# Kernel optimization log

Measured on AMD Instinct MI355X. Metric: run time of the kernel, lower is better.

Reference implementation:

```python
import jax, jax.numpy as jnp
import numpy as np

IN, H, OUT, B = 1024, 4096, 1, 4096


def setup_inputs() -> dict:
    key = jax.random.key(0)
    ks = jax.random.split(key, 20)
    sx = 1.0 / np.sqrt(IN)
    sh = 1.0 / np.sqrt(H)
    d = {
        "x": jax.random.normal(ks[0], (B, IN), jnp.float32),
        "hidden": jax.random.normal(ks[1], (B, H), jnp.float32),
        "cell": jax.random.normal(ks[2], (B, H), jnp.float32),
        # input projections (Linear(input_size, h_size)), weight [H, IN], bias [H]
        "Wx_i": jax.random.normal(ks[3], (H, IN), jnp.float32) * sx,
        "Wx_f": jax.random.normal(ks[4], (H, IN), jnp.float32) * sx,
        "Wx_o": jax.random.normal(ks[5], (H, IN), jnp.float32) * sx,
        "Wx_c": jax.random.normal(ks[6], (H, IN), jnp.float32) * sx,
        "bx_i": jax.random.normal(ks[7], (H,), jnp.float32) * sx,
        "bx_f": jax.random.normal(ks[8], (H,), jnp.float32) * sx,
        "bx_o": jax.random.normal(ks[9], (H,), jnp.float32) * sx,
        "bx_c": jax.random.normal(ks[10], (H,), jnp.float32) * sx,
        # hidden projections (Linear(h_size, h_size, bias=False)), weight [H, H]
        "Wh_i": jax.random.normal(ks[11], (H, H), jnp.float32) * sh,
        "Wh_f": jax.random.normal(ks[12], (H, H), jnp.float32) * sh,
        "Wh_o": jax.random.normal(ks[13], (H, H), jnp.float32) * sh,
        "Wh_c": jax.random.normal(ks[14], (H, H), jnp.float32) * sh,
        # output head Linear(h_size, out_size)
        "Wy": jax.random.normal(ks[15], (OUT, H), jnp.float32) * sh,
        "by": jax.random.normal(ks[16], (OUT,), jnp.float32) * sh,
    }
    return d


def reference(x, hidden, cell,
              Wx_i, Wx_f, Wx_o, Wx_c,
              bx_i, bx_f, bx_o, bx_c,
              Wh_i, Wh_f, Wh_o, Wh_c,
              Wy, by):
    # single LSTM step, batched over leading dim
    i = jax.nn.sigmoid(x @ Wx_i.T + bx_i + hidden @ Wh_i.T)
    f = jax.nn.sigmoid(x @ Wx_f.T + bx_f + hidden @ Wh_f.T)
    o = jax.nn.sigmoid(x @ Wx_o.T + bx_o + hidden @ Wh_o.T)
    c_til = jnp.tanh(x @ Wx_c.T + bx_c + hidden @ Wh_c.T)
    c_new = f * cell + i * c_til
    h_new = o * jnp.tanh(c_new)
    y_hat = h_new @ Wy.T + by  # [B, OUT]
    return y_hat
```

## Files before the change

kernel.cpp:

```cpp
#include <hip/hip_runtime.h>
#include <stdint.h>

#define IN_ 1024
#define H_  4096
#define B_  4096
#define K_  5120
#define NT_ 80

typedef short bf16x8 __attribute__((ext_vector_type(8)));
typedef float f32x4  __attribute__((ext_vector_type(4)));

__device__ __forceinline__ unsigned short f2bf(float x) {
    union { float f; uint32_t u; } v; v.f = x;
    return (unsigned short)((v.u + 0x7FFFu + ((v.u >> 16) & 1u)) >> 16);
}
__device__ __forceinline__ float bf2f(uint32_t u16) {
    union { uint32_t u; float f; } v; v.u = u16 << 16; return v.f;
}

__global__ __launch_bounds__(256) void cvt_cat(
    const float* __restrict__ s1, const float* __restrict__ s2,
    unsigned short* __restrict__ dst)
{
    int idx = blockIdx.x * 256 + threadIdx.x;
    int r = idx / (K_ / 4);
    int c = (idx % (K_ / 4)) * 4;
    float4 v;
    if (c < IN_) v = *(const float4*)(s1 + (size_t)r * IN_ + c);
    else         v = *(const float4*)(s2 + (size_t)r * H_ + (c - IN_));
    ushort4 o = { f2bf(v.x), f2bf(v.y), f2bf(v.z), f2bf(v.w) };
    *(ushort4*)(dst + (size_t)r * K_ + c) = o;
}

__device__ __forceinline__ int swz(int row) { return ((row >> 1) & 3) << 4; }

__global__ __launch_bounds__(512, 2) void gemm_gate8(
    const unsigned short* __restrict__ A,
    const unsigned short* __restrict__ W,
    const float* __restrict__ bias,
    unsigned short* __restrict__ P)
{
    __shared__ __align__(16) char ldsb[131072];

    const int tid  = threadIdx.x;
    const int wid  = tid >> 6;
    const int lane = tid & 63;

    const int wg = (blockIdx.x & 7) * 32 + (blockIdx.x >> 3);
    const int mt = wg & 15, nt = wg >> 4;
    const int bm = mt * 256, bn = nt * 256;

    const int wm = wid >> 2;
    const int wn = wid & 3;

    const int l15 = lane & 15;
    const int c0  = (lane >> 4) << 4;

    const int q0  = wid * 64 + lane;
    const int r0  = q0 >> 2;
    const int cb0 = ((q0 & 3) << 4) ^ swz(r0);
    const int r1  = r0 + 128;
    const int cb1 = ((q0 & 3) << 4) ^ swz(r1);

    f32x4 acc[8][4];
#pragma unroll
    for (int i = 0; i < 8; ++i)
#pragma unroll
        for (int j = 0; j < 4; ++j) acc[i][j] = (f32x4){0.f, 0.f, 0.f, 0.f};

    auto stage = [&](int isB, int ksel, int tau) {
        if (tau >= NT_) tau -= 2;
        const int kbase = tau * 64 + ksel * 32;
        const int chunk = (tau & 1) * 65536 + isB * 32768 + ksel * 16384;
        const unsigned short* src = isB ? W : A;
        const int gb = isB ? bn : bm;
        __builtin_amdgcn_global_load_lds(
            (const __attribute__((address_space(1))) void*)(src + (size_t)(gb + r0) * K_ + kbase + (cb0 >> 1)),
            (__attribute__((address_space(3))) void*)(ldsb + chunk + wid * 1024), 16, 0, 0);
        __builtin_amdgcn_global_load_lds(
            (const __attribute__((address_space(1))) void*)(src + (size_t)(gb + r1) * K_ + kbase + (cb1 >> 1)),
            (__attribute__((address_space(3))) void*)(ldsb + chunk + 8192 + wid * 1024), 16, 0, 0);
    };

    stage(0, 0, 0); stage(1, 0, 0);
    stage(0, 1, 0); stage(1, 1, 0);
    stage(0, 0, 1); stage(1, 0, 1);
    asm volatile("s_waitcnt vmcnt(8)" ::: "memory");
    __builtin_amdgcn_s_barrier();

    for (int T = 0; T < NT_; ++T) {
        const char* base = ldsb + (T & 1) * 65536;
#pragma unroll
        for (int p = 0; p < 2; ++p) {
            const char* Ab = base + p * 16384;
            const char* Bb = base + 32768 + p * 16384;

            bf16x8 a[8], b[4];
#pragma unroll
            for (int mi = 0; mi < 8; ++mi) {
                const int row = wm * 128 + mi * 16 + l15;
                a[mi] = *(const bf16x8*)(Ab + row * 64 + (c0 ^ swz(row)));
            }
#pragma unroll
            for (int ni = 0; ni < 4; ++ni) {
                const int row = wn * 64 + ni * 16 + l15;
                b[ni] = *(const bf16x8*)(Bb + row * 64 + (c0 ^ swz(row)));
            }

            if (p == 0) { stage(0, 1, T + 1); stage(1, 1, T + 1); }
            else        { stage(0, 0, T + 2); stage(1, 0, T + 2); }

            asm volatile("s_waitcnt vmcnt(8)" ::: "memory");
            __builtin_amdgcn_s_barrier();
            asm volatile("s_waitcnt lgkmcnt(0)" ::: "memory");
            __builtin_amdgcn_sched_barrier(0);
            __builtin_amdgcn_s_setprio(1);
#pragma unroll
            for (int mi = 0; mi < 8; ++mi)
#pragma unroll
                for (int ni = 0; ni < 4; ++ni)
                    acc[mi][ni] = __builtin_amdgcn_mfma_f32_16x16x32_bf16(
                        a[mi], b[ni], acc[mi][ni], 0, 0, 0);
            __builtin_amdgcn_s_setprio(0);
            __builtin_amdgcn_s_barrier();
        }
    }

#pragma unroll
    for (int ni = 0; ni < 4; ++ni) {
        const int col = bn + wn * 64 + ni * 16 + l15;
        const float bv = bias[col];
#pragma unroll
        for (int mi = 0; mi < 8; ++mi) {
            const int row0 = bm + wm * 128 + mi * 16 + (lane >> 4) * 4;
#pragma unroll
            for (int r = 0; r < 4; ++r)
                P[(size_t)(row0 + r) * H_ + col] = f2bf(acc[mi][ni][r] + bv);
        }
    }
}

__global__ __launch_bounds__(256) void gates_gemv(
    const unsigned short* __restrict__ Pi, const unsigned short* __restrict__ Pf,
    const unsigned short* __restrict__ Po, const unsigned short* __restrict__ Pc,
    const float* __restrict__ cell, const float* __restrict__ Wy,
    const float* __restrict__ by, float* __restrict__ y)
{
    const int b = blockIdx.x;
    const int t = threadIdx.x;
    const size_t base = (size_t)b * H_;
    float part = 0.f;

#pragma unroll
    for (int j = 0; j < 4; ++j) {
        const int h = j * 1024 + t * 4;
        const uint2 ri = *(const uint2*)(Pi + base + h);
        const uint2 rf = *(const uint2*)(Pf + base + h);
        const uint2 ro = *(const uint2*)(Po + base + h);
        const uint2 rc = *(const uint2*)(Pc + base + h);
        const float4 cv = *(const float4*)(cell + base + h);
        const float4 wv = *(const float4*)(Wy + h);

        const uint32_t zi[4] = { ri.x & 0xffffu, ri.x >> 16, ri.y & 0xffffu, ri.y >> 16 };
        const uint32_t zf[4] = { rf.x & 0xffffu, rf.x >> 16, rf.y & 0xffffu, rf.y >> 16 };
        const uint32_t zo[4] = { ro.x & 0xffffu, ro.x >> 16, ro.y & 0xffffu, ro.y >> 16 };
        const uint32_t zc[4] = { rc.x & 0xffffu, rc.x >> 16, rc.y & 0xffffu, rc.y >> 16 };
        const float cc[4] = { cv.x, cv.y, cv.z, cv.w };
        const float ww[4] = { wv.x, wv.y, wv.z, wv.w };
#pragma unroll
        for (int e = 0; e < 4; ++e) {
            const float ig = 1.f / (1.f + __expf(-bf2f(zi[e])));
            const float fg = 1.f / (1.f + __expf(-bf2f(zf[e])));
            const float og = 1.f / (1.f + __expf(-bf2f(zo[e])));
            const float ct = tanhf(bf2f(zc[e]));
            const float cn = fg * cc[e] + ig * ct;
            const float hn = og * tanhf(cn);
            part += hn * ww[e];
        }
    }

#pragma unroll
    for (int off = 32; off > 0; off >>= 1) part += __shfl_down(part, off, 64);
    __shared__ float red[4];
    if ((t & 63) == 0) red[t >> 6] = part;
    __syncthreads();
    if (t == 0) y[b] = red[0] + red[1] + red[2] + red[3] + by[0];
}

extern "C" void kernel_launch(void* const* d_in, const int* in_sizes, int n_in,
                              void* d_out, int out_size, void* d_ws, size_t ws_size,
                              hipStream_t stream) {
    const float* x      = (const float*)d_in[0];
    const float* hidden = (const float*)d_in[1];
    const float* cell   = (const float*)d_in[2];
    const float* Wx[4]  = { (const float*)d_in[3], (const float*)d_in[4],
                            (const float*)d_in[5], (const float*)d_in[6] };
    const float* bx[4]  = { (const float*)d_in[7], (const float*)d_in[8],
                            (const float*)d_in[9], (const float*)d_in[10] };
    const float* Wh[4]  = { (const float*)d_in[11], (const float*)d_in[12],
                            (const float*)d_in[13], (const float*)d_in[14] };
    const float* Wy     = (const float*)d_in[15];
    const float* by     = (const float*)d_in[16];
    float* y = (float*)d_out;

    unsigned short* Ab = (unsigned short*)d_ws;
    unsigned short* Wb = Ab + (size_t)B_ * K_;
    unsigned short* Pg[4];
    {
        unsigned short* p0 = Wb + (size_t)H_ * K_;
        for (int g = 0; g < 4; ++g) Pg[g] = p0 + (size_t)g * B_ * H_;
    }

    const int cvt_grid = (B_ * (K_ / 4)) / 256;
    cvt_cat<<<cvt_grid, 256, 0, stream>>>(x, hidden, Ab);

    for (int g = 0; g < 4; ++g) {
        cvt_cat<<<cvt_grid, 256, 0, stream>>>(Wx[g], Wh[g], Wb);
        gemm_gate8<<<256, 512, 0, stream>>>(Ab, Wb, bx[g], Pg[g]);
    }

    gates_gemv<<<B_, 256, 0, stream>>>(Pg[0], Pg[1], Pg[2], Pg[3], cell, Wy, by, y);
}
```

Measured before the change: 764.7 us.

## Restructure GEMM main loop into M-quarter phases with finer-grained LDS staging

The GEMM main loop now walks each 64-wide K tile in four M-quarter phases. Each phase loads A fragments for 32 rows across both K halves and reuses B fragments that are loaded once per tile. Global-to-LDS staging is spread across the phases: A for the next tile is issued early and B one tile further ahead, with adjusted vmcnt/lgkmcnt waits. The aim is to interleave loads with MFMA work more finely and use fewer registers per phase, at the cost of more barriers per tile and a more fragile prefetch ordering.

Measured after the change: 741.8 us. -3.0%, faster.

```diff
diff --git a/kernel.cpp b/kernel.cpp
--- a/kernel.cpp
+++ b/kernel.cpp
@@ -69,7 +69,7 @@
         for (int j = 0; j < 4; ++j) acc[i][j] = (f32x4){0.f, 0.f, 0.f, 0.f};
 
     auto stage = [&](int isB, int ksel, int tau) {
-        if (tau >= NT_) tau -= 2;
+        if (tau >= NT_) tau = NT_ - 2 + (tau & 1);
         const int kbase = tau * 64 + ksel * 32;
         const int chunk = (tau & 1) * 65536 + isB * 32768 + ksel * 16384;
         const unsigned short* src = isB ? W : A;
@@ -82,47 +82,69 @@
             (__attribute__((address_space(3))) void*)(ldsb + chunk + 8192 + wid * 1024), 16, 0, 0);
     };
 
-    stage(0, 0, 0); stage(1, 0, 0);
-    stage(0, 1, 0); stage(1, 1, 0);
-    stage(0, 0, 1); stage(1, 0, 1);
-    asm volatile("s_waitcnt vmcnt(8)" ::: "memory");
+    stage(0, 0, 0); stage(0, 1, 0); stage(1, 0, 0); stage(1, 1, 0);
+    stage(1, 0, 1); stage(1, 1, 1);
+    asm volatile("s_waitcnt vmcnt(4)" ::: "memory");
     __builtin_amdgcn_s_barrier();
 
-    for (int T = 0; T < NT_; ++T) {
-        const char* base = ldsb + (T & 1) * 65536;
-#pragma unroll
-        for (int p = 0; p < 2; ++p) {
-            const char* Ab = base + p * 16384;
-            const char* Bb = base + 32768 + p * 16384;
-
-            bf16x8 a[8], b[4];
-#pragma unroll
-            for (int mi = 0; mi < 8; ++mi) {
-                const int row = wm * 128 + mi * 16 + l15;
-                a[mi] = *(const bf16x8*)(Ab + row * 64 + (c0 ^ swz(row)));
+    for (int i = 0; i < NT_ / 2; ++i) {
+        const int T0 = 2 * i;
+#pragma unroll
+        for (int half = 0; half < 2; ++half) {
+            const char* base  = ldsb + half * 65536;
+            const char* Abase = base;
+            const char* Bbase = base + 32768;
+
+            bf16x8 b[2][4];
+#pragma unroll
+            for (int q = 0; q < 4; ++q) {
+                bf16x8 a[2][2];
+#pragma unroll
+                for (int kh = 0; kh < 2; ++kh)
+#pragma unroll
+                    for (int mi = 0; mi < 2; ++mi) {
+                        const int row = wm * 128 + q * 32 + mi * 16 + l15;
+                        a[kh][mi] = *(const bf16x8*)(Abase + kh * 16384 + row * 64 + (c0 ^ swz(row)));
+                    }
+                if (q == 0) {
+#pragma unroll
+                    for (int kh = 0; kh < 2; ++kh)
+#pragma unroll
+                        for (int ni = 0; ni < 4; ++ni) {
+                            const int row = wn * 64 + ni * 16 + l15;
+                            b[kh][ni] = *(const bf16x8*)(Bbase + kh * 16384 + row * 64 + (c0 ^ swz(row)));
+                        }
+                }
+
+                if (half == 0) {
+                    if      (q == 0) stage(0, 0, T0 + 1);
+                    else if (q == 1) stage(0, 1, T0 + 1);
+                    else if (q == 2) stage(1, 0, T0 + 2);
+                    else             stage(1, 1, T0 + 2);
+                } else {
+                    if      (q == 0) stage(0, 0, T0 + 2);
+                    else if (q == 1) stage(0, 1, T0 + 2);
+                    else if (q == 2) stage(1, 0, T0 + 3);
+                    else             stage(1, 1, T0 + 3);
+                }
+
+                if (q == 0) asm volatile("s_waitcnt lgkmcnt(8)" ::: "memory");
+                if (q == 3) asm volatile("s_waitcnt vmcnt(4)" ::: "memory");
+                __builtin_amdgcn_s_barrier();
+                asm volatile("s_waitcnt lgkmcnt(0)" ::: "memory");
+                __builtin_amdgcn_sched_barrier(0);
+                __builtin_amdgcn_s_setprio(1);
+#pragma unroll
+                for (int kh = 0; kh < 2; ++kh)
+#pragma unroll
+                    for (int mi = 0; mi < 2; ++mi)
+#pragma unroll
+                        for (int ni = 0; ni < 4; ++ni)
+                            acc[q * 2 + mi][ni] = __builtin_amdgcn_mfma_f32_16x16x32_bf16(
+                                a[kh][mi], b[kh][ni], acc[q * 2 + mi][ni], 0, 0, 0);
+                __builtin_amdgcn_s_setprio(0);
+                __builtin_amdgcn_s_barrier();
             }
-#pragma unroll
-            for (int ni = 0; ni < 4; ++ni) {
-                const int row = wn * 64 + ni * 16 + l15;
-                b[ni] = *(const bf16x8*)(Bb + row * 64 + (c0 ^ swz(row)));
-            }
-
-            if (p == 0) { stage(0, 1, T + 1); stage(1, 1, T + 1); }
-            else        { stage(0, 0, T + 2); stage(1, 0, T + 2); }
-
-            asm volatile("s_waitcnt vmcnt(8)" ::: "memory");
-            __builtin_amdgcn_s_barrier();
-            asm volatile("s_waitcnt lgkmcnt(0)" ::: "memory");
-            __builtin_amdgcn_sched_barrier(0);
-            __builtin_amdgcn_s_setprio(1);
-#pragma unroll
-            for (int mi = 0; mi < 8; ++mi)
-#pragma unroll
-                for (int ni = 0; ni < 4; ++ni)
-                    acc[mi][ni] = __builtin_amdgcn_mfma_f32_16x16x32_bf16(
-                        a[mi], b[ni], acc[mi][ni], 0, 0, 0);
-            __builtin_amdgcn_s_setprio(0);
-            __builtin_amdgcn_s_barrier();
         }
     }
 
```
